# Optimization experiments

Measured on AMD Instinct MI355X. Metric: run time of the kernel, lower is better.

The kernel has to match this reference:

```python
import jax, jax.numpy as jnp
import numpy as np

# Static DAG: input -> L hidden layers of K nodes (dense between layers) -> output.
B, WIDTH, K, L = 262144, 64, 4, 4


def _linear_init(key, shape, fan_in):
    # matches nn.Linear default: U(-1/sqrt(fan_in), 1/sqrt(fan_in))
    bound = 1.0 / np.sqrt(fan_in)
    return jax.random.uniform(key, shape, jnp.float32, -bound, bound)


def setup_inputs() -> dict:
    key = jax.random.key(0)
    ks = jax.random.split(key, 9)
    x = jax.random.normal(ks[0], (B, WIDTH), jnp.float32)
    # input node -> first hidden layer (K edges)
    W_in = _linear_init(ks[1], (K, WIDTH, WIDTH), WIDTH)
    b_in = _linear_init(ks[2], (K, WIDTH), WIDTH)
    # between hidden layers: (L-1) transitions, K*K edges each; [pred, node, out, in]
    W_mid = _linear_init(ks[3], (L - 1, K, K, WIDTH, WIDTH), WIDTH)
    b_mid = _linear_init(ks[4], (L - 1, K, K, WIDTH), WIDTH)
    # last hidden layer -> output node (K edges)
    W_out = _linear_init(ks[5], (K, WIDTH, WIDTH), WIDTH)
    b_out = _linear_init(ks[6], (K, WIDTH), WIDTH)
    return {"x": x, "W_in": W_in, "b_in": b_in, "W_mid": W_mid,
            "b_mid": b_mid, "W_out": W_out, "b_out": b_out}


def _l2_normalize(t):
    # torch.linalg.norm(t) with no dim: Frobenius norm over the WHOLE tensor
    return t / jnp.linalg.norm(t)


def reference(x, W_in, b_in, W_mid, b_mid, W_out, b_out):
    # input node -> layer 1: each node k gets a single edge Linear, then normalize
    h = jnp.einsum('bw,kvw->kbv', x, W_in) + b_in[:, None, :]  # [K,B,W]
    h = jax.vmap(_l2_normalize)(h)
    # hidden -> hidden transitions: node v sums over its K predecessor edges
    for l in range(L - 1):  # small fixed structural loop over layers
        pre = jnp.einsum('pbw,pkvw->kbv', h, W_mid[l]) + b_mid[l].sum(axis=0)[:, None, :]
        h = jax.vmap(_l2_normalize)(pre)
    # last layer -> output node: sum K edge outputs, normalize
    out = jnp.einsum('pbw,pvw->bv', h, W_out) + b_out.sum(axis=0)
    return _l2_normalize(out)
```

## Files before the change

kernel.cpp:

```cpp
#include <hip/hip_runtime.h>


#define BF 262144.0f

#define OFF_G   0
#define OFF_S   4096
#define OFF_P0  8192
#define OFF_P1  73728
#define OFF_C0  139264
#define OFF_C1  140288
#define OFF_MO  141312
#define OFF_CO  145408

typedef __attribute__((ext_vector_type(8))) short bf16x8;
typedef __attribute__((ext_vector_type(4))) float f32x4;

__device__ __forceinline__ unsigned short f2bf(float f) {
  unsigned u = __builtin_bit_cast(unsigned, f);
  u += 0x7FFF + ((u >> 16) & 1);
  return (unsigned short)(u >> 16);
}

__device__ __forceinline__ bf16x8 cvt8(f32x4 a, f32x4 b, float s) {
  bf16x8 t;
#pragma unroll
  for (int j = 0; j < 4; j++) {
    t[j]     = (short)f2bf(a[j] * s);
    t[j + 4] = (short)f2bf(b[j] * s);
  }
  return t;
}

__global__ __launch_bounds__(256) void kG(const float* __restrict__ x,
                                          float* __restrict__ Gpart) {
  __shared__ __align__(16) unsigned short xts[4][4][16][8];
  __shared__ float sred[256][4];
  const int tid = threadIdx.x;
  const int lane = tid & 63, mt = tid >> 6;
  const int col = lane & 15, q = lane >> 4;
  const int row0 = tid >> 4;
  const int cf0  = (tid & 15) * 4;

  f32x4 acc[4];
#pragma unroll
  for (int nt = 0; nt < 4; nt++) acc[nt] = (f32x4){0.f, 0.f, 0.f, 0.f};
  float s0 = 0.f, s1 = 0.f, s2 = 0.f, s3 = 0.f;

  const float* bx = x + (long)blockIdx.x * 32768;
  f32x4 r0 = *(const f32x4*)(bx + tid * 4);
  f32x4 r1 = *(const f32x4*)(bx + 1024 + tid * 4);

  for (int c = 0; c < 16; c++) {
    __syncthreads();
    s0 += r0[0] + r1[0]; s1 += r0[1] + r1[1];
    s2 += r0[2] + r1[2]; s3 += r0[3] + r1[3];
#pragma unroll
    for (int j = 0; j < 4; j++) {
      const int cf = cf0 + j;
      xts[cf >> 4][row0 >> 3][cf & 15][row0 & 7]        = f2bf(r0[j]);
      xts[cf >> 4][2 + (row0 >> 3)][cf & 15][row0 & 7]  = f2bf(r1[j]);
    }
    f32x4 r0n = r0, r1n = r1;
    if (c < 15) {
      r0n = *(const f32x4*)(bx + (c + 1) * 2048 + tid * 4);
      r1n = *(const f32x4*)(bx + (c + 1) * 2048 + 1024 + tid * 4);
    }
    __syncthreads();
    const bf16x8 af = *(const bf16x8*)xts[mt][q][col];
#pragma unroll
    for (int nt = 0; nt < 4; nt++) {
      const bf16x8 bfr = *(const bf16x8*)xts[nt][q][col];
      acc[nt] = __builtin_amdgcn_mfma_f32_16x16x32_bf16(af, bfr, acc[nt], 0, 0, 0);
    }
    r0 = r0n; r1 = r1n;
  }

  float* myp = Gpart + (long)blockIdx.x * 4160;
#pragma unroll
  for (int nt = 0; nt < 4; nt++)
#pragma unroll
    for (int r = 0; r < 4; r++)
      myp[(mt * 16 + q * 4 + r) * 64 + nt * 16 + col] = acc[nt][r];

  sred[tid][0] = s0; sred[tid][1] = s1; sred[tid][2] = s2; sred[tid][3] = s3;
  __syncthreads();
  if (tid < 64) {
    float t = 0.f;
#pragma unroll
    for (int k2 = 0; k2 < 16; k2++) t += sred[(tid >> 2) + 16 * k2][tid & 3];
    myp[4096 + tid] = t;
  }
}

__global__ __launch_bounds__(256) void kGred(const float* __restrict__ Gpart,
                                             float* __restrict__ G,
                                             float* __restrict__ s) {
  __shared__ float red[4][64];
  const int tid = threadIdx.x;
  const int e = blockIdx.x * 64 + (tid & 63);
  const int quarter = tid >> 6;
  float acc = 0.f;
#pragma unroll 4
  for (int j = 0; j < 128; j++)
    acc += Gpart[(long)(quarter * 128 + j) * 4160 + e];
  red[quarter][tid & 63] = acc;
  __syncthreads();
  if (tid < 64) {
    const float t = red[0][tid] + red[1][tid] + red[2][tid] + red[3][tid];
    const int ee = blockIdx.x * 64 + tid;
    if (ee < 4096) G[ee] = t;
    else           s[ee - 4096] = t;
  }
}

__global__ __launch_bounds__(256) void kLayer(const float* __restrict__ Tsrc,
                                              const float* __restrict__ csrc,
                                              const float* __restrict__ Wm,
                                              const float* __restrict__ bm,
                                              const float* __restrict__ G,
                                              const float* __restrict__ s,
                                              float* __restrict__ Pout,
                                              float* __restrict__ cpout,
                                              const int KN, const int first) {
  __shared__ float Tl[64][68], Gl[64][68], Wl[64][68];
  __shared__ float red[256];
  __shared__ __align__(16) float cl[64], sl[64];
  const int tid = threadIdx.x;
  const int p = blockIdx.x / KN, kk = blockIdx.x % KN;

#pragma unroll
  for (int m = 0; m < 16; m++) {
    const int li = m * 256 + tid;
    const int r = li >> 6, cc = li & 63;
    float tv;
    if (first) tv = Tsrc[p * 4096 + li];
    else tv = Tsrc[p * 4096 + li] + Tsrc[(4 + p) * 4096 + li] +
              Tsrc[(8 + p) * 4096 + li] + Tsrc[(12 + p) * 4096 + li];
    Tl[r][cc] = tv;
    Gl[r][cc] = G[li];
    Wl[r][cc] = Wm[(long)(p * KN + kk) * 4096 + li];
  }
  if (tid < 64) {
    float cv;
    if (first) cv = csrc[p * 64 + tid];
    else cv = csrc[p * 64 + tid] + csrc[(4 + p) * 64 + tid] +
              csrc[(8 + p) * 64 + tid] + csrc[(12 + p) * 64 + tid];
    cl[tid] = cv;
    sl[tid] = s[tid];
  }
  __syncthreads();

  const int v = tid >> 2, iq = tid & 3;
  {
    f32x4 Tr[16];
#pragma unroll
    for (int u4 = 0; u4 < 16; u4++) Tr[u4] = *(const f32x4*)&Tl[v][u4 * 4];
    float part = 0.f;
    for (int i = 0; i < 16; i++) {
      const int ii = iq * 16 + i;
      float gv = 0.f;
#pragma unroll
      for (int u4 = 0; u4 < 16; u4++) {
        const f32x4 g = *(const f32x4*)&Gl[ii][u4 * 4];
        gv += g[0] * Tr[u4][0] + g[1] * Tr[u4][1] + g[2] * Tr[u4][2] + g[3] * Tr[u4][3];
      }
      part += Tl[v][ii] * gv;
    }
    if (iq == 0) {
      float sd = 0.f;
#pragma unroll
      for (int u4 = 0; u4 < 16; u4++) {
        const f32x4 sv = *(const f32x4*)&sl[u4 * 4];
        sd += sv[0] * Tr[u4][0] + sv[1] * Tr[u4][1] + sv[2] * Tr[u4][2] + sv[3] * Tr[u4][3];
      }
      part += cl[v] * (2.f * sd + BF * cl[v]);
    }
    red[tid] = part;
  }
  __syncthreads();
  for (int st = 128; st > 0; st >>= 1) {
    if (tid < st) red[tid] += red[tid + st];
    __syncthreads();
  }
  const float inv = 1.0f / sqrtf(red[0]);

  {
    const int vo = tid >> 3;
    const int w8 = (tid & 7) * 8;
    float a0[8], a1[8];
#pragma unroll
    for (int j = 0; j < 8; j++) { a0[j] = 0.f; a1[j] = 0.f; }
    for (int ub = 0; ub < 4; ub++) {
      f32x4 wr0[4], wr1[4];
#pragma unroll
      for (int j = 0; j < 4; j++) {
        wr0[j] = *(const f32x4*)&Wl[vo][ub * 16 + j * 4];
        wr1[j] = *(const f32x4*)&Wl[vo + 32][ub * 16 + j * 4];
      }
#pragma unroll
      for (int uu = 0; uu < 16; uu++) {
        const int u = ub * 16 + uu;
        const f32x4 t0 = *(const f32x4*)&Tl[u][w8];
        const f32x4 t1 = *(const f32x4*)&Tl[u][w8 + 4];
        const float w0 = wr0[uu >> 2][uu & 3];
        const float w1 = wr1[uu >> 2][uu & 3];
#pragma unroll
        for (int j = 0; j < 4; j++) {
          a0[j]     += w0 * t0[j]; a0[j + 4] += w0 * t1[j];
          a1[j]     += w1 * t0[j]; a1[j + 4] += w1 * t1[j];
        }
      }
    }
    float* po = Pout + (long)(p * KN + kk) * 4096;
    f32x4 o;
#pragma unroll
    for (int j = 0; j < 4; j++) o[j] = inv * a0[j];
    *(f32x4*)(po + vo * 64 + w8) = o;
#pragma unroll
    for (int j = 0; j < 4; j++) o[j] = inv * a0[j + 4];
    *(f32x4*)(po + vo * 64 + w8 + 4) = o;
#pragma unroll
    for (int j = 0; j < 4; j++) o[j] = inv * a1[j];
    *(f32x4*)(po + (vo + 32) * 64 + w8) = o;
#pragma unroll
    for (int j = 0; j < 4; j++) o[j] = inv * a1[j + 4];
    *(f32x4*)(po + (vo + 32) * 64 + w8 + 4) = o;
  }

  if (tid < 64) {
    float pc = 0.f;
#pragma unroll
    for (int u4 = 0; u4 < 16; u4++) {
      const f32x4 wv = *(const f32x4*)&Wl[tid][u4 * 4];
      pc += wv[0] * cl[u4 * 4] + wv[1] * cl[u4 * 4 + 1] +
            wv[2] * cl[u4 * 4 + 2] + wv[3] * cl[u4 * 4 + 3];
    }
    cpout[(p * KN + kk) * 64 + tid] = inv * pc + bm[(long)(p * KN + kk) * 64 + tid];
  }
}

__global__ __launch_bounds__(256) void kNorm(const float* __restrict__ Psrc,
                                             const float* __restrict__ csrc,
                                             const float* __restrict__ G,
                                             const float* __restrict__ s,
                                             float* __restrict__ MoS,
                                             float* __restrict__ coS) {
  __shared__ float Tl[64][68], Gl[64][68];
  __shared__ float red[256];
  __shared__ __align__(16) float cl[64], sl[64];
  const int tid = threadIdx.x;
#pragma unroll
  for (int m = 0; m < 16; m++) {
    const int li = m * 256 + tid;
    const int r = li >> 6, cc = li & 63;
    Tl[r][cc] = Psrc[li] + Psrc[4096 + li] + Psrc[8192 + li] + Psrc[12288 + li];
    Gl[r][cc] = G[li];
  }
  if (tid < 64) {
    cl[tid] = csrc[tid] + csrc[64 + tid] + csrc[128 + tid] + csrc[192 + tid];
    sl[tid] = s[tid];
  }
  __syncthreads();

  const int v = tid >> 2, iq = tid & 3;
  f32x4 Tr[16];
#pragma unroll
  for (int u4 = 0; u4 < 16; u4++) Tr[u4] = *(const f32x4*)&Tl[v][u4 * 4];
  float part = 0.f;
  for (int i = 0; i < 16; i++) {
    const int ii = iq * 16 + i;
    float gv = 0.f;
#pragma unroll
    for (int u4 = 0; u4 < 16; u4++) {
      const f32x4 g = *(const f32x4*)&Gl[ii][u4 * 4];
      gv += g[0] * Tr[u4][0] + g[1] * Tr[u4][1] + g[2] * Tr[u4][2] + g[3] * Tr[u4][3];
    }
    part += Tl[v][ii] * gv;
  }
  if (iq == 0) {
    float sd = 0.f;
#pragma unroll
    for (int u4 = 0; u4 < 16; u4++) {
      const f32x4 sv = *(const f32x4*)&sl[u4 * 4];
      sd += sv[0] * Tr[u4][0] + sv[1] * Tr[u4][1] + sv[2] * Tr[u4][2] + sv[3] * Tr[u4][3];
    }
    part += cl[v] * (2.f * sd + BF * cl[v]);
  }
  red[tid] = part;
  __syncthreads();
  for (int st = 128; st > 0; st >>= 1) {
    if (tid < st) red[tid] += red[tid + st];
    __syncthreads();
  }
  const float inv = 1.0f / sqrtf(red[0]);

#pragma unroll
  for (int m = 0; m < 16; m++) {
    const int li = m * 256 + tid;
    MoS[li] = inv * Tl[li >> 6][li & 63];
  }
  if (tid < 64) coS[tid] = inv * cl[tid];
}

__global__ __launch_bounds__(256) void kApply(const float* __restrict__ x,
                                              const float* __restrict__ MoS,
                                              const float* __restrict__ coS,
                                              float* __restrict__ out) {
  const int tid = threadIdx.x, lane = tid & 63, vt = tid >> 6;
  const int col = lane & 15, q = lane >> 4;

  bf16x8 bfr[2];
  const float* mr = MoS + (vt * 16 + col) * 64 + q * 8;
  bfr[0] = cvt8(*(const f32x4*)mr, *(const f32x4*)(mr + 4), 1.f);
  bfr[1] = cvt8(*(const f32x4*)(mr + 32), *(const f32x4*)(mr + 36), 1.f);
  const float cf = coS[vt * 16 + col];

  for (int t = 0; t < 16; t++) {
    const int b0 = (blockIdx.x * 16 + t) * 16;
    const float* xr = x + (long)(b0 + col) * 64 + q * 8;
    const bf16x8 a0 = cvt8(*(const f32x4*)xr, *(const f32x4*)(xr + 4), 1.f);
    const bf16x8 a1 = cvt8(*(const f32x4*)(xr + 32), *(const f32x4*)(xr + 36), 1.f);
    f32x4 acc = (f32x4){0.f, 0.f, 0.f, 0.f};
    acc = __builtin_amdgcn_mfma_f32_16x16x32_bf16(a0, bfr[0], acc, 0, 0, 0);
    acc = __builtin_amdgcn_mfma_f32_16x16x32_bf16(a1, bfr[1], acc, 0, 0, 0);
#pragma unroll
    for (int r = 0; r < 4; r++)
      out[(long)(b0 + q * 4 + r) * 64 + vt * 16 + col] = acc[r] + cf;
  }
}

extern "C" void kernel_launch(void* const* d_in, const int* in_sizes, int n_in,
                              void* d_out, int out_size, void* d_ws, size_t ws_size,
                              hipStream_t stream) {
  const float* x    = (const float*)d_in[0];
  const float* Win  = (const float*)d_in[1];
  const float* bin  = (const float*)d_in[2];
  const float* Wmid = (const float*)d_in[3];
  const float* bmid = (const float*)d_in[4];
  const float* Wout = (const float*)d_in[5];
  const float* bout = (const float*)d_in[6];
  float* out = (float*)d_out;
  float* ws  = (float*)d_ws;
  float* Gpart = out;

  kG   <<<512, 256, 0, stream>>>(x, Gpart);
  kGred<<<65, 256, 0, stream>>>(Gpart, ws + OFF_G, ws + OFF_S);
  kLayer<<<16, 256, 0, stream>>>(Win, bin, Wmid, bmid,
                                 ws + OFF_G, ws + OFF_S, ws + OFF_P0, ws + OFF_C0, 4, 1);
  kLayer<<<16, 256, 0, stream>>>(ws + OFF_P0, ws + OFF_C0, Wmid + 65536, bmid + 1024,
                                 ws + OFF_G, ws + OFF_S, ws + OFF_P1, ws + OFF_C1, 4, 0);
  kLayer<<<16, 256, 0, stream>>>(ws + OFF_P1, ws + OFF_C1, Wmid + 131072, bmid + 2048,
                                 ws + OFF_G, ws + OFF_S, ws + OFF_P0, ws + OFF_C0, 4, 0);
  kLayer<<<4, 256, 0, stream>>>(ws + OFF_P0, ws + OFF_C0, Wout, bout,
                                 ws + OFF_G, ws + OFF_S, ws + OFF_P1, ws + OFF_C1, 1, 0);
  kNorm<<<1, 256, 0, stream>>>(ws + OFF_P1, ws + OFF_C1, ws + OFF_G, ws + OFF_S,
                               ws + OFF_MO, ws + OFF_CO);
  kApply<<<1024, 256, 0, stream>>>(x, ws + OFF_MO, ws + OFF_CO, out);
}
```

Measured before the change: 266.0 us.

## Use split-bf16 MFMA for small 64x64 matmuls in layer and norm kernels

Replaces the scalar FP32 loops in kLayer and kNorm with MFMA bf16 matrix ops. Each FP32 operand is split into high and low bf16 parts, and three MFMA products are taken to keep near-FP32 accuracy. G moves into registers, and W is read from global memory again for the bias-propagation dot product. This targets the serial FMA cost of the tiny per-block 64x64 products. It adds an extra transpose and split pass, two syncs, and some accuracy risk.

Result: faster. 233.9 us (-12.1%).

```diff
diff --git a/kernel.cpp b/kernel.cpp
--- a/kernel.cpp
+++ b/kernel.cpp
@@ -19,6 +19,10 @@
   unsigned u = __builtin_bit_cast(unsigned, f);
   u += 0x7FFF + ((u >> 16) & 1);
   return (unsigned short)(u >> 16);
+}
+__device__ __forceinline__ float bf2f(unsigned short h) {
+  unsigned u = ((unsigned)h) << 16;
+  return __builtin_bit_cast(float, u);
 }
 
 __device__ __forceinline__ bf16x8 cvt8(f32x4 a, f32x4 b, float s) {
@@ -122,11 +126,22 @@
                                               float* __restrict__ Pout,
                                               float* __restrict__ cpout,
                                               const int KN, const int first) {
-  __shared__ float Tl[64][68], Gl[64][68], Wl[64][68];
+  __shared__ float Tf[64][68];
+  __shared__ __align__(16) unsigned short Tth[64][68], Ttl[64][68];
+  __shared__ __align__(16) unsigned short Wh[64][68], Wlo[64][68];
   __shared__ float red[256];
   __shared__ __align__(16) float cl[64], sl[64];
   const int tid = threadIdx.x;
   const int p = blockIdx.x / KN, kk = blockIdx.x % KN;
+  const int lane = tid & 63, it = tid >> 6;
+  const int col = lane & 15, quad = lane >> 4;
+
+  float Greg[4][4];
+#pragma unroll
+  for (int ut = 0; ut < 4; ut++)
+#pragma unroll
+    for (int r = 0; r < 4; r++)
+      Greg[ut][r] = G[(it * 16 + quad * 4 + r) * 64 + ut * 16 + col];
 
 #pragma unroll
   for (int m = 0; m < 16; m++) {
@@ -136,9 +151,11 @@
     if (first) tv = Tsrc[p * 4096 + li];
     else tv = Tsrc[p * 4096 + li] + Tsrc[(4 + p) * 4096 + li] +
               Tsrc[(8 + p) * 4096 + li] + Tsrc[(12 + p) * 4096 + li];
-    Tl[r][cc] = tv;
-    Gl[r][cc] = G[li];
-    Wl[r][cc] = Wm[(long)(p * KN + kk) * 4096 + li];
+    Tf[r][cc] = tv;
+    const float wv = Wm[(long)(p * KN + kk) * 4096 + li];
+    const unsigned short wh = f2bf(wv);
+    Wh[r][cc] = wh;
+    Wlo[r][cc] = f2bf(wv - bf2f(wh));
   }
   if (tid < 64) {
     float cv;
@@ -150,33 +167,54 @@
   }
   __syncthreads();
 
-  const int v = tid >> 2, iq = tid & 3;
   {
-    f32x4 Tr[16];
-#pragma unroll
-    for (int u4 = 0; u4 < 16; u4++) Tr[u4] = *(const f32x4*)&Tl[v][u4 * 4];
-    float part = 0.f;
-    for (int i = 0; i < 16; i++) {
-      const int ii = iq * 16 + i;
-      float gv = 0.f;
-#pragma unroll
-      for (int u4 = 0; u4 < 16; u4++) {
-        const f32x4 g = *(const f32x4*)&Gl[ii][u4 * 4];
-        gv += g[0] * Tr[u4][0] + g[1] * Tr[u4][1] + g[2] * Tr[u4][2] + g[3] * Tr[u4][3];
+    const int tc = tid >> 2;
+    const int rb = (tid & 3) * 16;
+#pragma unroll
+    for (int j = 0; j < 16; j++) {
+      const float tv = Tf[rb + j][tc];
+      const unsigned short h = f2bf(tv);
+      Tth[tc][rb + j] = h;
+      Ttl[tc][rb + j] = f2bf(tv - bf2f(h));
+    }
+  }
+  __syncthreads();
+
+  float qp = 0.f;
+  {
+    f32x4 dq[4];
+#pragma unroll
+    for (int ut = 0; ut < 4; ut++) dq[ut] = (f32x4){0.f, 0.f, 0.f, 0.f};
+#pragma unroll
+    for (int ks = 0; ks < 2; ks++) {
+      const bf16x8 ah = *(const bf16x8*)&Tth[it * 16 + col][ks * 32 + quad * 8];
+      const bf16x8 al = *(const bf16x8*)&Ttl[it * 16 + col][ks * 32 + quad * 8];
+#pragma unroll
+      for (int ut = 0; ut < 4; ut++) {
+        const bf16x8 bh = *(const bf16x8*)&Tth[ut * 16 + col][ks * 32 + quad * 8];
+        const bf16x8 bl = *(const bf16x8*)&Ttl[ut * 16 + col][ks * 32 + quad * 8];
+        dq[ut] = __builtin_amdgcn_mfma_f32_16x16x32_bf16(ah, bh, dq[ut], 0, 0, 0);
+        dq[ut] = __builtin_amdgcn_mfma_f32_16x16x32_bf16(ah, bl, dq[ut], 0, 0, 0);
+        dq[ut] = __builtin_amdgcn_mfma_f32_16x16x32_bf16(al, bh, dq[ut], 0, 0, 0);
       }
-      part += Tl[v][ii] * gv;
-    }
-    if (iq == 0) {
-      float sd = 0.f;
-#pragma unroll
-      for (int u4 = 0; u4 < 16; u4++) {
-        const f32x4 sv = *(const f32x4*)&sl[u4 * 4];
-        sd += sv[0] * Tr[u4][0] + sv[1] * Tr[u4][1] + sv[2] * Tr[u4][2] + sv[3] * Tr[u4][3];
-      }
-      part += cl[v] * (2.f * sd + BF * cl[v]);
-    }
-    red[tid] = part;
-  }
+    }
+#pragma unroll
+    for (int ut = 0; ut < 4; ut++)
+#pragma unroll
+      for (int r = 0; r < 4; r++)
+        qp += dq[ut][r] * Greg[ut][r];
+  }
+  if (tid < 64) {
+    float sd = 0.f;
+#pragma unroll
+    for (int u4 = 0; u4 < 16; u4++) {
+      const f32x4 tv = *(const f32x4*)&Tf[tid][u4 * 4];
+      const f32x4 sv = *(const f32x4*)&sl[u4 * 4];
+      sd += sv[0] * tv[0] + sv[1] * tv[1] + sv[2] * tv[2] + sv[3] * tv[3];
+    }
+    qp += cl[tid] * (2.f * sd + BF * cl[tid]);
+  }
+  red[tid] = qp;
   __syncthreads();
   for (int st = 128; st > 0; st >>= 1) {
     if (tid < st) red[tid] += red[tid + st];
@@ -185,53 +223,36 @@
   const float inv = 1.0f / sqrtf(red[0]);
 
   {
-    const int vo = tid >> 3;
-    const int w8 = (tid & 7) * 8;
-    float a0[8], a1[8];
-#pragma unroll
-    for (int j = 0; j < 8; j++) { a0[j] = 0.f; a1[j] = 0.f; }
-    for (int ub = 0; ub < 4; ub++) {
-      f32x4 wr0[4], wr1[4];
-#pragma unroll
-      for (int j = 0; j < 4; j++) {
-        wr0[j] = *(const f32x4*)&Wl[vo][ub * 16 + j * 4];
-        wr1[j] = *(const f32x4*)&Wl[vo + 32][ub * 16 + j * 4];
+    f32x4 dc[4];
+#pragma unroll
+    for (int nt = 0; nt < 4; nt++) dc[nt] = (f32x4){0.f, 0.f, 0.f, 0.f};
+#pragma unroll
+    for (int ks = 0; ks < 2; ks++) {
+      const bf16x8 awh = *(const bf16x8*)&Wh[it * 16 + col][ks * 32 + quad * 8];
+      const bf16x8 awl = *(const bf16x8*)&Wlo[it * 16 + col][ks * 32 + quad * 8];
+#pragma unroll
+      for (int nt = 0; nt < 4; nt++) {
+        const bf16x8 bh = *(const bf16x8*)&Tth[nt * 16 + col][ks * 32 + quad * 8];
+        const bf16x8 bl = *(const bf16x8*)&Ttl[nt * 16 + col][ks * 32 + quad * 8];
+        dc[nt] = __builtin_amdgcn_mfma_f32_16x16x32_bf16(awh, bh, dc[nt], 0, 0, 0);
+        dc[nt] = __builtin_amdgcn_mfma_f32_16x16x32_bf16(awh, bl, dc[nt], 0, 0, 0);
+        dc[nt] = __builtin_amdgcn_mfma_f32_16x16x32_bf16(awl, bh, dc[nt], 0, 0, 0);
       }
-#pragma unroll
-      for (int uu = 0; uu < 16; uu++) {
-        const int u = ub * 16 + uu;
-        const f32x4 t0 = *(const f32x4*)&Tl[u][w8];
-        const f32x4 t1 = *(const f32x4*)&Tl[u][w8 + 4];
-        const float w0 = wr0[uu >> 2][uu & 3];
-        const float w1 = wr1[uu >> 2][uu & 3];
-#pragma unroll
-        for (int j = 0; j < 4; j++) {
-          a0[j]     += w0 * t0[j]; a0[j + 4] += w0 * t1[j];
-          a1[j]     += w1 * t0[j]; a1[j + 4] += w1 * t1[j];
-        }
-      }
     }
     float* po = Pout + (long)(p * KN + kk) * 4096;
-    f32x4 o;
-#pragma unroll
-    for (int j = 0; j < 4; j++) o[j] = inv * a0[j];
-    *(f32x4*)(po + vo * 64 + w8) = o;
-#pragma unroll
-    for (int j = 0; j < 4; j++) o[j] = inv * a0[j + 4];
-    *(f32x4*)(po + vo * 64 + w8 + 4) = o;
-#pragma unroll
-    for (int j = 0; j < 4; j++) o[j] = inv * a1[j];
-    *(f32x4*)(po + (vo + 32) * 64 + w8) = o;
-#pragma unroll
-    for (int j = 0; j < 4; j++) o[j] = inv * a1[j + 4];
-    *(f32x4*)(po + (vo + 32) * 64 + w8 + 4) = o;
-  }
-
-  if (tid < 64) {
+#pragma unroll
+    for (int nt = 0; nt < 4; nt++)
+#pragma unroll
+      for (int r = 0; r < 4; r++)
+        po[(it * 16 + quad * 4 + r) * 64 + nt * 16 + col] = inv * dc[nt][r];
+  }
+
+  if (tid < 64) {
+    const float* wg = Wm + (long)(p * KN + kk) * 4096 + tid * 64;
     float pc = 0.f;
 #pragma unroll
     for (int u4 = 0; u4 < 16; u4++) {
-      const f32x4 wv = *(const f32x4*)&Wl[tid][u4 * 4];
+      const f32x4 wv = *(const f32x4*)(wg + u4 * 4);
       pc += wv[0] * cl[u4 * 4] + wv[1] * cl[u4 * 4 + 1] +
             wv[2] * cl[u4 * 4 + 2] + wv[3] * cl[u4 * 4 + 3];
     }
@@ -245,16 +266,25 @@
                                              const float* __restrict__ s,
                                              float* __restrict__ MoS,
                                              float* __restrict__ coS) {
-  __shared__ float Tl[64][68], Gl[64][68];
+  __shared__ float Tf[64][68];
+  __shared__ __align__(16) unsigned short Tth[64][68], Ttl[64][68];
   __shared__ float red[256];
   __shared__ __align__(16) float cl[64], sl[64];
   const int tid = threadIdx.x;
+  const int lane = tid & 63, it = tid >> 6;
+  const int col = lane & 15, quad = lane >> 4;
+
+  float Greg[4][4];
+#pragma unroll
+  for (int ut = 0; ut < 4; ut++)
+#pragma unroll
+    for (int r = 0; r < 4; r++)
+      Greg[ut][r] = G[(it * 16 + quad * 4 + r) * 64 + ut * 16 + col];
+
 #pragma unroll
   for (int m = 0; m < 16; m++) {
     const int li = m * 256 + tid;
-    const int r = li >> 6, cc = li & 63;
-    Tl[r][cc] = Psrc[li] + Psrc[4096 + li] + Psrc[8192 + li] + Psrc[12288 + li];
-    Gl[r][cc] = G[li];
+    Tf[li >> 6][li & 63] = Psrc[li] + Psrc[4096 + li] + Psrc[8192 + li] + Psrc[12288 + li];
   }
   if (tid < 64) {
     cl[tid] = csrc[tid] + csrc[64 + tid] + csrc[128 + tid] + csrc[192 + tid];
@@ -262,31 +292,54 @@
   }
   __syncthreads();
 
-  const int v = tid >> 2, iq = tid & 3;
-  f32x4 Tr[16];
-#pragma unroll
-  for (int u4 = 0; u4 < 16; u4++) Tr[u4] = *(const f32x4*)&Tl[v][u4 * 4];
-  float part = 0.f;
-  for (int i = 0; i < 16; i++) {
-    const int ii = iq * 16 + i;
-    float gv = 0.f;
+  {
+    const int tc = tid >> 2;
+    const int rb = (tid & 3) * 16;
+#pragma unroll
+    for (int j = 0; j < 16; j++) {
+      const float tv = Tf[rb + j][tc];
+      const unsigned short h = f2bf(tv);
+      Tth[tc][rb + j] = h;
+      Ttl[tc][rb + j] = f2bf(tv - bf2f(h));
+    }
+  }
+  __syncthreads();
+
+  float qp = 0.f;
+  {
+    f32x4 dq[4];
+#pragma unroll
+    for (int ut = 0; ut < 4; ut++) dq[ut] = (f32x4){0.f, 0.f, 0.f, 0.f};
+#pragma unroll
+    for (int ks = 0; ks < 2; ks++) {
+      const bf16x8 ah = *(const bf16x8*)&Tth[it * 16 + col][ks * 32 + quad * 8];
+      const bf16x8 al = *(const bf16x8*)&Ttl[it * 16 + col][ks * 32 + quad * 8];
+#pragma unroll
+      for (int ut = 0; ut < 4; ut++) {
+        const bf16x8 bh = *(const bf16x8*)&Tth[ut * 16 + col][ks * 32 + quad * 8];
+        const bf16x8 bl = *(const bf16x8*)&Ttl[ut * 16 + col][ks * 32 + quad * 8];
+        dq[ut] = __builtin_amdgcn_mfma_f32_16x16x32_bf16(ah, bh, dq[ut], 0, 0, 0);
+        dq[ut] = __builtin_amdgcn_mfma_f32_16x16x32_bf16(ah, bl, dq[ut], 0, 0, 0);
+        dq[ut] = __builtin_amdgcn_mfma_f32_16x16x32_bf16(al, bh, dq[ut], 0, 0, 0);
+      }
+    }
+#pragma unroll
+    for (int ut = 0; ut < 4; ut++)
+#pragma unroll
+      for (int r = 0; r < 4; r++)
+        qp += dq[ut][r] * Greg[ut][r];
+  }
+  if (tid < 64) {
+    float sd = 0.f;
 #pragma unroll
     for (int u4 = 0; u4 < 16; u4++) {
-      const f32x4 g = *(const f32x4*)&Gl[ii][u4 * 4];
-      gv += g[0] * Tr[u4][0] + g[1] * Tr[u4][1] + g[2] * Tr[u4][2] + g[3] * Tr[u4][3];
-    }
-    part += Tl[v][ii] * gv;
-  }
-  if (iq == 0) {
-    float sd = 0.f;
-#pragma unroll
-    for (int u4 = 0; u4 < 16; u4++) {
+      const f32x4 tv = *(const f32x4*)&Tf[tid][u4 * 4];
       const f32x4 sv = *(const f32x4*)&sl[u4 * 4];
-      sd += sv[0] * Tr[u4][0] + sv[1] * Tr[u4][1] + sv[2] * Tr[u4][2] + sv[3] * Tr[u4][3];
-    }
-    part += cl[v] * (2.f * sd + BF * cl[v]);
-  }
-  red[tid] = part;
+      sd += sv[0] * tv[0] + sv[1] * tv[1] + sv[2] * tv[2] + sv[3] * tv[3];
+    }
+    qp += cl[tid] * (2.f * sd + BF * cl[tid]);
+  }
+  red[tid] = qp;
   __syncthreads();
   for (int st = 128; st > 0; st >>= 1) {
     if (tid < st) red[tid] += red[tid + st];
@@ -297,7 +350,7 @@
 #pragma unroll
   for (int m = 0; m < 16; m++) {
     const int li = m * 256 + tid;
-    MoS[li] = inv * Tl[li >> 6][li & 63];
+    MoS[li] = inv * Tf[li >> 6][li & 63];
   }
   if (tid < 64) coS[tid] = inv * cl[tid];
 }
```
